# Performance work log

Measured on AMD Instinct MI355X. Metric: run time of the kernel, lower is better.

The kernel has to match this reference:

```python
import jax, jax.numpy as jnp
import numpy as np

D_MODEL = 1024
N_HEADS = 16
HEAD_DIM = D_MODEL // N_HEADS
Q_PROJ = D_MODEL // 2
KV_PROJ = D_MODEL
INIT_SCALE = 0.02
EPS = 1e-5


def _ln(x, g, b):
    mu = jnp.mean(x, axis=-1, keepdims=True)
    var = jnp.mean(jnp.square(x - mu), axis=-1, keepdims=True)
    return (x - mu) * jax.lax.rsqrt(var + EPS) * g + b


def setup_inputs() -> dict:
    key = jax.random.key(0)
    ks = jax.random.split(key, 8)
    B, S = 2, 2048
    x = jax.random.normal(ks[0], (B, S, D_MODEL), dtype=jnp.float32)
    W_dq = INIT_SCALE * jax.random.normal(ks[1], (D_MODEL, Q_PROJ), dtype=jnp.float32)
    W_uq = INIT_SCALE * jax.random.normal(ks[2], (Q_PROJ, D_MODEL), dtype=jnp.float32)
    W_dkv = INIT_SCALE * jax.random.normal(ks[3], (D_MODEL, KV_PROJ), dtype=jnp.float32)
    W_ukv = INIT_SCALE * jax.random.normal(ks[4], (KV_PROJ, 2 * D_MODEL), dtype=jnp.float32)
    wo = INIT_SCALE * jax.random.normal(ks[5], (D_MODEL, D_MODEL), dtype=jnp.float32)
    return {
        "x": x,
        "W_dq": W_dq, "W_uq": W_uq,
        "q_ln_g": jnp.ones((Q_PROJ,), jnp.float32), "q_ln_b": jnp.zeros((Q_PROJ,), jnp.float32),
        "W_dkv": W_dkv, "W_ukv": W_ukv,
        "kv_ln_g": jnp.ones((KV_PROJ,), jnp.float32), "kv_ln_b": jnp.zeros((KV_PROJ,), jnp.float32),
        "preq_g": jnp.ones((D_MODEL,), jnp.float32), "preq_b": jnp.zeros((D_MODEL,), jnp.float32),
        "prekv_g": jnp.ones((D_MODEL,), jnp.float32), "prekv_b": jnp.zeros((D_MODEL,), jnp.float32),
        "wo": wo,
    }


def reference(x, W_dq, W_uq, q_ln_g, q_ln_b, W_dkv, W_ukv, kv_ln_g, kv_ln_b,
              preq_g, preq_b, prekv_g, prekv_b, wo):
    B, S, D = x.shape
    H, dh = N_HEADS, HEAD_DIM
    # Q path: pre-norm -> low-rank down -> LN -> up
    x_q = _ln(x, preq_g, preq_b)
    cq = _ln(x_q @ W_dq, q_ln_g, q_ln_b)            # [B,S,D/2]
    Q = (cq @ W_uq).reshape(B, S, H, dh)             # [B,S,H,dh]
    Q = Q / jnp.sqrt(jnp.asarray(dh, x.dtype))
    # KV path: pre-norm -> compress -> LN -> up, split into K,V
    x_kv = _ln(x, prekv_g, prekv_b)
    ckv = _ln(x_kv @ W_dkv, kv_ln_g, kv_ln_b)        # [B,S,D]
    KV = ckv @ W_ukv                                 # [B,S,2D]
    K, V = jnp.split(KV, 2, axis=-1)
    K = K.reshape(B, S, H, dh)
    V = V.reshape(B, S, H, dh)
    # causal attention (scores materialized as in original)
    scores = jnp.einsum('bqhd,bkhd->bhqk', Q, K)     # [B,H,S,S]
    causal = jnp.tril(jnp.ones((S, S), dtype=bool))  # True where allowed
    scores = jnp.where(causal[None, None], scores, jnp.asarray(-jnp.inf, scores.dtype))
    attn = jax.nn.softmax(scores, axis=-1)
    out = jnp.einsum('bhqk,bkhd->bqhd', attn, V).reshape(B, S, D)
    return out @ wo.T
```

## Files before the change

kernel.cpp:

```cpp
#include <hip/hip_runtime.h>
#include <hip/hip_bf16.h>

#define SEQ   2048
#define BATCH 2
#define NROWS 4096
#define DM    1024
#define NHEAD 16
#define DH    64
#define QP    512
#define KVP   1024
#define CH    8

typedef unsigned short us;
typedef ushort4 us4;
using bf16x8 = __attribute__((ext_vector_type(8))) __bf16;
using f32x4  = __attribute__((ext_vector_type(4))) float;

__device__ __forceinline__ us f2bf(float f) {
  union { __hip_bfloat16 h; us u; } cv;
  cv.h = __float2bfloat16(f);
  return cv.u;
}
__device__ __forceinline__ float bf2f(us u) {
  union { unsigned int u32; float f; } cv;
  cv.u32 = ((unsigned int)u) << 16;
  return cv.f;
}
__device__ __forceinline__ float loadp(const void* p, long i, int isbf) {
  return isbf ? bf2f(((const us*)p)[i]) : ((const float*)p)[i];
}
__device__ __forceinline__ void async16(const void* g, void* l) {
  __builtin_amdgcn_global_load_lds((__attribute__((address_space(1))) void*)g,
                                   (__attribute__((address_space(3))) void*)l,
                                   16, 0, 0);
}
__device__ __forceinline__ unsigned cvtpk(float lo, float hi) {
  unsigned r;
  asm("v_cvt_pk_bf16_f32 %0, %1, %2" : "=v"(r) : "v"(lo), "v"(hi));
  return r;
}

__global__ void detect_dtype(const us* __restrict__ xu, int* __restrict__ flag) {
  __shared__ int red[256];
  const int tid = threadIdx.x;
  int cnt = 0;
  for (int i = tid; i < 4096; i += 256) {
    const int e = (xu[i] >> 7) & 0xff;
    if (e == 0 || (e >= 100 && e <= 134)) cnt++;
  }
  red[tid] = cnt;
  __syncthreads();
  for (int s = 128; s; s >>= 1) {
    if (tid < s) red[tid] += red[tid + s];
    __syncthreads();
  }
  if (tid == 0) *flag = (red[0] >= 3900) ? 1 : 0;
}

struct TD { const void* in; us* out; int R, C, nt, trans; };

__global__ __launch_bounds__(256) void stage0(
    TD t0, TD t1, TD t2, TD t3, TD t4,
    float4* __restrict__ zp, int n4,
    const void* __restrict__ xin,
    const void* __restrict__ g1, const void* __restrict__ b1,
    const void* __restrict__ g2, const void* __restrict__ b2,
    us* __restrict__ out1, us* __restrict__ out2,
    const int* __restrict__ flag)
{
  __shared__ us tile[32][33];
  __shared__ float red[8];
  __shared__ float musd[2];
  const int tid = threadIdx.x;
  const int isbf = *flag;
  int lin = blockIdx.x;

  if (lin < 5120) {
    TD t = t0;
    if (lin >= t.nt) { lin -= t.nt; t = t1;
      if (lin >= t.nt) { lin -= t.nt; t = t2;
        if (lin >= t.nt) { lin -= t.nt; t = t3;
          if (lin >= t.nt) { lin -= t.nt; t = t4; } } } }
    const int ntx = t.C >> 5;
    const int by = lin / ntx, bx = lin - by * ntx;
    const int tx = tid & 31, ty = tid >> 5;
    const long r0 = (long)by * 32, c0 = (long)bx * 32;
    if (t.trans) {
#pragma unroll
      for (int i = 0; i < 32; i += 8)
        tile[ty + i][tx] = isbf ? ((const us*)t.in)[(r0 + ty + i) * t.C + c0 + tx]
                                : f2bf(((const float*)t.in)[(r0 + ty + i) * t.C + c0 + tx]);
      __syncthreads();
#pragma unroll
      for (int i = 0; i < 32; i += 8)
        t.out[(c0 + ty + i) * t.R + r0 + tx] = tile[tx][ty + i];
    } else {
#pragma unroll
      for (int i = 0; i < 32; i += 8)
        t.out[(r0 + ty + i) * t.C + c0 + tx] =
            isbf ? ((const us*)t.in)[(r0 + ty + i) * t.C + c0 + tx]
                 : f2bf(((const float*)t.in)[(r0 + ty + i) * t.C + c0 + tx]);
    }
    return;
  }
  if (lin < 6144) {
    const float4 z = {0.f, 0.f, 0.f, 0.f};
    for (int i = (lin - 5120) * 256 + tid; i < n4; i += 1024 * 256) zp[i] = z;
    return;
  }
  const long row = lin - 6144;
  float v[4];
  float s = 0.f, s2 = 0.f;
#pragma unroll
  for (int i = 0; i < 4; i++) {
    const long c = tid + i * 256;
    const float t = loadp(xin, row * 1024 + c, isbf);
    v[i] = t; s += t; s2 += t * t;
  }
#pragma unroll
  for (int off = 32; off > 0; off >>= 1) {
    s  += __shfl_down(s,  off);
    s2 += __shfl_down(s2, off);
  }
  const int wave = tid >> 6, lane = tid & 63;
  if (lane == 0) { red[wave] = s; red[4 + wave] = s2; }
  __syncthreads();
  if (tid == 0) {
    const float ts = red[0] + red[1] + red[2] + red[3];
    const float t2 = red[4] + red[5] + red[6] + red[7];
    const float mu = ts * (1.f / 1024.f);
    const float var = t2 * (1.f / 1024.f) - mu * mu;
    musd[0] = mu; musd[1] = rsqrtf(var + 1e-5f);
  }
  __syncthreads();
  const float mu = musd[0], rs = musd[1];
#pragma unroll
  for (int i = 0; i < 4; i++) {
    const long c = tid + i * 256;
    const float nrm = (v[i] - mu) * rs;
    out1[row * 1024 + c] = f2bf(nrm * loadp(g1, c, isbf) + loadp(b1, c, isbf));
    out2[row * 1024 + c] = f2bf(nrm * loadp(g2, c, isbf) + loadp(b2, c, isbf));
  }
}

template<int C>
__device__ __forceinline__ void ln_body(const us* __restrict__ in,
                                        const void* __restrict__ g, const void* __restrict__ b,
                                        us* __restrict__ out, long row, int tid, int isbf) {
  constexpr int NP = C / 256;
  float v[NP];
  float s = 0.f, s2 = 0.f;
#pragma unroll
  for (int i = 0; i < NP; i++) {
    const float t = bf2f(in[row * C + tid + i * 256]);
    v[i] = t; s += t; s2 += t * t;
  }
#pragma unroll
  for (int off = 32; off > 0; off >>= 1) {
    s  += __shfl_down(s,  off);
    s2 += __shfl_down(s2, off);
  }
  __shared__ float red[8];
  __shared__ float musd[2];
  const int wave = tid >> 6, lane = tid & 63;
  if (lane == 0) { red[wave] = s; red[4 + wave] = s2; }
  __syncthreads();
  if (tid == 0) {
    const float ts = red[0] + red[1] + red[2] + red[3];
    const float t2 = red[4] + red[5] + red[6] + red[7];
    const float mu = ts * (1.f / C);
    const float var = t2 * (1.f / C) - mu * mu;
    musd[0] = mu; musd[1] = rsqrtf(var + 1e-5f);
  }
  __syncthreads();
  const float mu = musd[0], rs = musd[1];
#pragma unroll
  for (int i = 0; i < NP; i++) {
    const long c = tid + i * 256;
    out[row * C + c] = f2bf((v[i] - mu) * rs * loadp(g, c, isbf) + loadp(b, c, isbf));
  }
}

__global__ __launch_bounds__(256) void ln_rows_pair(
    const us* __restrict__ inq, const void* __restrict__ qg, const void* __restrict__ qb,
    us* __restrict__ outq,
    const us* __restrict__ inkv, const void* __restrict__ kvg, const void* __restrict__ kvb,
    us* __restrict__ outkv,
    const int* __restrict__ flag)
{
  const int isbf = *flag;
  if (blockIdx.x < NROWS)
    ln_body<512>(inq, qg, qb, outq, blockIdx.x, threadIdx.x, isbf);
  else
    ln_body<1024>(inkv, kvg, kvb, outkv, blockIdx.x - NROWS, threadIdx.x, isbf);
}

struct GD { const us* A; const us* Bt; void* C; int N, K, nxs; float scale; int omode; };

__global__ __launch_bounds__(256) void gemm_mt(GD g0, GD g1, int nb0,
                                               const int* __restrict__ flag) {
  __shared__ us As[2][128 * 32];
  __shared__ us Bs[2][128 * 32];
  GD g;
  int lin = blockIdx.x;
  if (lin < nb0) g = g0; else { g = g1; lin -= nb0; }
  const int by = lin >> g.nxs;
  const int bx = lin - (by << g.nxs);
  const int N = g.N, K = g.K;

  const int tid  = threadIdx.x;
  const int lane = tid & 63;
  const int wave = tid >> 6;
  const int n16  = lane & 15;
  const int quad = lane >> 4;
  const long m0 = (long)by * 128;
  const long n0 = (long)bx * 128;
  const int wm = (wave >> 1) * 64;
  const int wn = (wave & 1) * 64;

  const f32x4 zero = {0.f, 0.f, 0.f, 0.f};
  f32x4 acc[4][4];
#pragma unroll
  for (int i = 0; i < 4; i++)
#pragma unroll
    for (int j = 0; j < 4; j++) acc[i][j] = zero;

  const int srow = tid >> 2;
  const int scol = (tid & 3) * 8;
  const us* Ag0 = g.A  + (m0 + srow) * K + scol;
  const us* Ag1 = g.A  + (m0 + 64 + srow) * K + scol;
  const us* Bg0 = g.Bt + (n0 + srow) * K + scol;
  const us* Bg1 = g.Bt + (n0 + 64 + srow) * K + scol;
  const int lds_off = srow * 32 + scol;

  for (int k0 = 0; k0 < K; k0 += 64) {
#pragma unroll
    for (int s = 0; s < 2; s++) {
      const int ks = k0 + s * 32;
      async16(Ag0 + ks, As[s] + lds_off);
      async16(Ag1 + ks, As[s] + 2048 + lds_off);
      async16(Bg0 + ks, Bs[s] + lds_off);
      async16(Bg1 + ks, Bs[s] + 2048 + lds_off);
    }
    __syncthreads();
#pragma unroll
    for (int s = 0; s < 2; s++) {
      bf16x8 af[4], bfv[4];
#pragma unroll
      for (int i = 0; i < 4; i++)
        af[i] = *(const bf16x8*)(As[s] + (wm + i * 16 + n16) * 32 + quad * 8);
#pragma unroll
      for (int j = 0; j < 4; j++)
        bfv[j] = *(const bf16x8*)(Bs[s] + (wn + j * 16 + n16) * 32 + quad * 8);
#pragma unroll
      for (int i = 0; i < 4; i++)
#pragma unroll
        for (int j = 0; j < 4; j++)
          acc[i][j] = __builtin_amdgcn_mfma_f32_16x16x32_bf16(af[i], bfv[j], acc[i][j], 0, 0, 0);
    }
    __syncthreads();
  }

  const bool obf = (g.omode == 1) || (g.omode == 2 && *flag != 0);
  float* Cf = (float*)g.C;
  us* Cb = (us*)g.C;
#pragma unroll
  for (int i = 0; i < 4; i++) {
    const long row = m0 + wm + i * 16 + quad * 4;
#pragma unroll
    for (int j = 0; j < 4; j++) {
      const long col = n0 + wn + j * 16 + n16;
#pragma unroll
      for (int r = 0; r < 4; r++) {
        const float v = acc[i][j][r] * g.scale;
        if (obf) Cb[(row + r) * N + col] = f2bf(v);
        else     Cf[(row + r) * N + col] = v;
      }
    }
  }
}

#define SWZ(row, col) ((row) * 64 + ((col) ^ (((row) & 7) << 3)))

__global__ __launch_bounds__(256, 4) void flash_attn(
    const us* __restrict__ Q, const us* __restrict__ KV,
    float* __restrict__ Oacc, float* __restrict__ Lacc)
{
  __shared__ us Ks[64 * 64];
  __shared__ us Vt[64 * 64];

  int lin = blockIdx.x;
  int qt = 31, nc = 0;
  for (; qt >= 0; --qt) { nc = (qt >> 3) + 1; if (lin < nc) break; lin -= nc; }
  const int chunk = lin;
  const int kt0 = chunk * CH;
  const int kt1 = min(kt0 + CH, qt + 1);

  const int h   = blockIdx.y;
  const int bb  = blockIdx.z;
  const int tid = threadIdx.x;
  const int lane = tid & 63;
  const int wave = tid >> 6;
  const int n16 = lane & 15;
  const int quad = lane >> 4;
  const int qbase = qt * 64;
  const long rowQ0 = (long)bb * SEQ;

  bf16x8 aq[2];
  {
    const long gq = (rowQ0 + qbase + wave * 16 + n16) * DM + h * DH;
    aq[0] = *(const bf16x8*)(Q + gq + quad * 8);
    aq[1] = *(const bf16x8*)(Q + gq + 32 + quad * 8);
  }

  const f32x4 zero = {0.f, 0.f, 0.f, 0.f};
  f32x4 oacc[4];
#pragma unroll
  for (int d = 0; d < 4; d++) oacc[d] = zero;
  float rsum = 0.f;

  const int kk_key = tid >> 3;
  const int kk_d8  = (tid & 7) * 8;
  const int vd  = tid & 63;
  const int vw  = tid >> 6;
  const int vkb = vw * 8;

  const us* kgb = KV + (rowQ0 + kk_key) * 2048 + h * DH + kk_d8;
  const us* vgb = KV + (rowQ0 + vw * 4) * 2048 + KVP + h * DH + vd;

  uint4 kpre0, kpre1;
  us vraw[16];
  auto loadKV = [&](int kt) {
    const us* kg = kgb + (long)kt * (64 * 2048);
    kpre0 = *(const uint4*)kg;
    kpre1 = *(const uint4*)(kg + 32 * 2048);
    const us* vg = vgb + (long)kt * (64 * 2048);
#pragma unroll
    for (int r = 0; r < 4; r++) {
      vraw[r]      = vg[r * 2048];
      vraw[4 + r]  = vg[(16 + r) * 2048];
      vraw[8 + r]  = vg[(32 + r) * 2048];
      vraw[12 + r] = vg[(48 + r) * 2048];
    }
  };
  loadKV(kt0);

  for (int kt = kt0; kt < kt1; kt++) {
    __syncthreads();
    *(uint4*)(Ks + SWZ(kk_key, kk_d8))      = kpre0;
    *(uint4*)(Ks + SWZ(kk_key + 32, kk_d8)) = kpre1;
    {
      uint4 p0, p1;
      p0.x = (unsigned)vraw[0]  | ((unsigned)vraw[1]  << 16);
      p0.y = (unsigned)vraw[2]  | ((unsigned)vraw[3]  << 16);
      p0.z = (unsigned)vraw[4]  | ((unsigned)vraw[5]  << 16);
      p0.w = (unsigned)vraw[6]  | ((unsigned)vraw[7]  << 16);
      p1.x = (unsigned)vraw[8]  | ((unsigned)vraw[9]  << 16);
      p1.y = (unsigned)vraw[10] | ((unsigned)vraw[11] << 16);
      p1.z = (unsigned)vraw[12] | ((unsigned)vraw[13] << 16);
      p1.w = (unsigned)vraw[14] | ((unsigned)vraw[15] << 16);
      *(uint4*)(Vt + SWZ(vd, vkb))      = p0;
      *(uint4*)(Vt + SWZ(vd, vkb + 32)) = p1;
    }
    __syncthreads();
    if (kt + 1 < kt1) loadKV(kt + 1);

    f32x4 sv[4];
#pragma unroll
    for (int j = 0; j < 4; j++) {
      const bf16x8 ak0 = *(const bf16x8*)(Ks + SWZ(j * 16 + n16, quad * 8));
      const bf16x8 ak1 = *(const bf16x8*)(Ks + SWZ(j * 16 + n16, 32 + quad * 8));
      f32x4 s = zero;
      s = __builtin_amdgcn_mfma_f32_16x16x32_bf16(ak0, aq[0], s, 0, 0, 0);
      s = __builtin_amdgcn_mfma_f32_16x16x32_bf16(ak1, aq[1], s, 0, 0, 0);
      sv[j] = s;
    }

    if (kt == qt) {
      const int qrl = wave * 16 + n16;
#pragma unroll
      for (int j = 0; j < 4; j++) {
        const int kl = j * 16 + quad * 4;
#pragma unroll
        for (int r = 0; r < 4; r++)
          sv[j][r] = (kl + r <= qrl) ? sv[j][r] : -1e30f;
      }
    }

    unsigned pep[4][2];
#pragma unroll
    for (int j = 0; j < 4; j++) {
      const float p0 = __builtin_amdgcn_exp2f(sv[j][0]);
      const float p1 = __builtin_amdgcn_exp2f(sv[j][1]);
      const float p2 = __builtin_amdgcn_exp2f(sv[j][2]);
      const float p3 = __builtin_amdgcn_exp2f(sv[j][3]);
      rsum += (p0 + p1) + (p2 + p3);
      pep[j][0] = cvtpk(p0, p1);
      pep[j][1] = cvtpk(p2, p3);
    }

    __builtin_amdgcn_s_setprio(1);
#pragma unroll
    for (int kc = 0; kc < 2; kc++) {
      union { bf16x8 v; unsigned u[4]; } apu;
      apu.u[0] = pep[2 * kc][0];
      apu.u[1] = pep[2 * kc][1];
      apu.u[2] = pep[2 * kc + 1][0];
      apu.u[3] = pep[2 * kc + 1][1];
#pragma unroll
      for (int d = 0; d < 4; d++) {
        const bf16x8 bv = *(const bf16x8*)(Vt + SWZ(d * 16 + n16, kc * 32 + quad * 8));
        oacc[d] = __builtin_amdgcn_mfma_f32_16x16x32_bf16(apu.v, bv, oacc[d], 0, 0, 0);
      }
    }
    __builtin_amdgcn_s_setprio(0);
  }

  rsum += __shfl_xor(rsum, 16);
  rsum += __shfl_xor(rsum, 32);

  const long rw0 = rowQ0 + qbase + wave * 16;
  if (quad == 0)
    atomicAdd(&Lacc[(rw0 + n16) * NHEAD + h], rsum);
#pragma unroll
  for (int r = 0; r < 4; r++) {
    float* dst = Oacc + (rw0 + quad * 4 + r) * DM + h * DH + n16;
#pragma unroll
    for (int d = 0; d < 4; d++)
      atomicAdd(dst + d * 16, oacc[d][r]);
  }
}

__global__ __launch_bounds__(256) void flash_combine(
    const float* __restrict__ Oacc, const float* __restrict__ Lacc,
    us* __restrict__ O)
{
  __shared__ float invl[NHEAD];
  const long row = blockIdx.x;
  const int tid = threadIdx.x;
  if (tid < NHEAD) invl[tid] = 1.f / Lacc[row * NHEAD + tid];
  __syncthreads();
#pragma unroll
  for (int i = 0; i < 4; i++) {
    const int col = tid + i * 256;
    O[row * DM + col] = f2bf(Oacc[row * DM + col] * invl[col >> 6]);
  }
}

extern "C" void kernel_launch(void* const* d_in, const int* in_sizes, int n_in,
                              void* d_out, int out_size, void* d_ws, size_t ws_size,
                              hipStream_t stream) {
  const void* x      = d_in[0];
  const void* Wdq    = d_in[1];
  const void* Wuq    = d_in[2];
  const void* qg     = d_in[3];
  const void* qb     = d_in[4];
  const void* Wdkv   = d_in[5];
  const void* Wukv   = d_in[6];
  const void* kvg    = d_in[7];
  const void* kvb    = d_in[8];
  const void* preqg  = d_in[9];
  const void* preqb  = d_in[10];
  const void* prekvg = d_in[11];
  const void* prekvb = d_in[12];
  const void* wo     = d_in[13];

  char* ws = (char*)d_ws;
  const long MB = 1 << 20;
  int* flag   = (int*)ws;
  us* wdq_t   = (us*)(ws + 1 * MB);
  us* wuq_t   = (us*)(ws + 2 * MB);
  us* wdkv_t  = (us*)(ws + 3 * MB);
  us* wukv_t  = (us*)(ws + 5 * MB);
  us* wo_c    = (us*)(ws + 9 * MB);
  us* xq      = (us*)(ws + 11 * MB);
  us* xkv     = (us*)(ws + 19 * MB);
  float* Oacc = (float*)(ws + 27 * MB);
  float* Lacc = (float*)(ws + 43 * MB);
  us* obuf    = (us*)(ws + 43 * MB + 256 * 1024);
  us* tq_bf   = obuf;
  us* cq      = (us*)(ws + 43 * MB + 256 * 1024 + 8 * MB);
  us* qbuf    = (us*)(ws + 43 * MB + 256 * 1024 + 12 * MB);
  us* tkv_bf  = qbuf;
  us* ckv     = (us*)(ws + 43 * MB + 256 * 1024 + 20 * MB);
  us* kv      = (us*)(ws + 43 * MB + 256 * 1024 + 28 * MB);

  detect_dtype<<<1, 256, 0, stream>>>((const us*)x, flag);

  {
    TD t0 = { Wdq,  wdq_t,  1024,  512,  512, 1 };
    TD t1 = { Wuq,  wuq_t,   512, 1024,  512, 1 };
    TD t2 = { Wdkv, wdkv_t, 1024, 1024, 1024, 1 };
    TD t3 = { Wukv, wukv_t, 1024, 2048, 2048, 1 };
    TD t4 = { wo,   wo_c,   1024, 1024, 1024, 0 };
    const int n4 = (16 * 1024 * 1024 + 256 * 1024) / 16;
    stage0<<<10240, 256, 0, stream>>>(t0, t1, t2, t3, t4,
                                      (float4*)Oacc, n4,
                                      x, preqg, preqb, prekvg, prekvb, xq, xkv, flag);
  }

  {
    GD g0 = { xq,  wdq_t,  tq_bf,   512, 1024, 2, 1.f, 1 };
    GD g1 = { xkv, wdkv_t, tkv_bf, 1024, 1024, 3, 1.f, 1 };
    gemm_mt<<<384, 256, 0, stream>>>(g0, g1, 128, flag);
  }

  ln_rows_pair<<<2 * NROWS, 256, 0, stream>>>(tq_bf, qg, qb, cq, tkv_bf, kvg, kvb, ckv, flag);

  {
    GD g0 = { cq,  wuq_t,  qbuf, 1024,  512, 3, 0.125f * 1.44269504f, 1 };
    GD g1 = { ckv, wukv_t, kv,   2048, 1024, 4, 1.f, 1 };
    gemm_mt<<<768, 256, 0, stream>>>(g0, g1, 256, flag);
  }

  flash_attn<<<dim3(80, NHEAD, BATCH), 256, 0, stream>>>(qbuf, kv, Oacc, Lacc);
  flash_combine<<<NROWS, 256, 0, stream>>>(Oacc, Lacc, obuf);

  {
    GD g0 = { obuf, wo_c, d_out, 1024, 1024, 3, 1.f, 2 };
    gemm_mt<<<256, 256, 0, stream>>>(g0, g0, 256, flag);
  }
}
```

Before: 271.3 us.

## Process 128 query rows per attention block and remap GEMM block order

The attention kernel now has each wave handle two 16-row query groups, so a block covers 128 query rows. Each K/V tile staged in shared memory is reused across twice as many queries, and the atomic partial-sum traffic per key is halved. The causal mask is applied per group only when a tile overlaps the diagonal. The GEMM kernel also permutes block indices in strides of eight, probably so neighbouring tiles land on the same chiplet for cache locality. The cost is higher register pressure, fewer blocks in the attention grid, and coarser causal load balance.

```diff
diff --git a/kernel.cpp b/kernel.cpp
--- a/kernel.cpp
+++ b/kernel.cpp
@@ -203,6 +203,10 @@
   __shared__ us Bs[2][128 * 32];
   GD g;
   int lin = blockIdx.x;
+  {
+    const int cpx = gridDim.x >> 3;
+    lin = (lin & 7) * cpx + (lin >> 3);
+  }
   if (lin < nb0) g = g0; else { g = g1; lin -= nb0; }
   const int by = lin >> g.nxs;
   const int bx = lin - (by << g.nxs);
@@ -290,11 +294,15 @@
   __shared__ us Vt[64 * 64];
 
   int lin = blockIdx.x;
-  int qt = 31, nc = 0;
-  for (; qt >= 0; --qt) { nc = (qt >> 3) + 1; if (lin < nc) break; lin -= nc; }
-  const int chunk = lin;
-  const int kt0 = chunk * CH;
-  const int kt1 = min(kt0 + CH, qt + 1);
+  int qt = 15, nkt = 0, nc = 0;
+  for (; qt >= 0; --qt) {
+    nkt = 2 * qt + 2;
+    nc = (nkt + 7) >> 3;
+    if (lin < nc) break;
+    lin -= nc;
+  }
+  const int kt0 = lin * CH;
+  const int kt1 = min(kt0 + CH, nkt);
 
   const int h   = blockIdx.y;
   const int bb  = blockIdx.z;
@@ -303,21 +311,24 @@
   const int wave = tid >> 6;
   const int n16 = lane & 15;
   const int quad = lane >> 4;
-  const int qbase = qt * 64;
+  const int qbase = qt * 128;
   const long rowQ0 = (long)bb * SEQ;
 
-  bf16x8 aq[2];
-  {
-    const long gq = (rowQ0 + qbase + wave * 16 + n16) * DM + h * DH;
-    aq[0] = *(const bf16x8*)(Q + gq + quad * 8);
-    aq[1] = *(const bf16x8*)(Q + gq + 32 + quad * 8);
+  bf16x8 aq[2][2];
+#pragma unroll
+  for (int g = 0; g < 2; g++) {
+    const long gq = (rowQ0 + qbase + wave * 32 + g * 16 + n16) * DM + h * DH;
+    aq[g][0] = *(const bf16x8*)(Q + gq + quad * 8);
+    aq[g][1] = *(const bf16x8*)(Q + gq + 32 + quad * 8);
   }
 
   const f32x4 zero = {0.f, 0.f, 0.f, 0.f};
-  f32x4 oacc[4];
-#pragma unroll
-  for (int d = 0; d < 4; d++) oacc[d] = zero;
-  float rsum = 0.f;
+  f32x4 oacc[2][4];
+#pragma unroll
+  for (int g = 0; g < 2; g++)
+#pragma unroll
+    for (int d = 0; d < 4; d++) oacc[g][d] = zero;
+  float rsum[2] = {0.f, 0.f};
 
   const int kk_key = tid >> 3;
   const int kk_d8  = (tid & 7) * 8;
@@ -365,69 +376,73 @@
     __syncthreads();
     if (kt + 1 < kt1) loadKV(kt + 1);
 
-    f32x4 sv[4];
+    const int kb = kt << 6;
+    unsigned pep[2][4][2];
+
 #pragma unroll
     for (int j = 0; j < 4; j++) {
       const bf16x8 ak0 = *(const bf16x8*)(Ks + SWZ(j * 16 + n16, quad * 8));
       const bf16x8 ak1 = *(const bf16x8*)(Ks + SWZ(j * 16 + n16, 32 + quad * 8));
-      f32x4 s = zero;
-      s = __builtin_amdgcn_mfma_f32_16x16x32_bf16(ak0, aq[0], s, 0, 0, 0);
-      s = __builtin_amdgcn_mfma_f32_16x16x32_bf16(ak1, aq[1], s, 0, 0, 0);
-      sv[j] = s;
-    }
-
-    if (kt == qt) {
-      const int qrl = wave * 16 + n16;
-#pragma unroll
-      for (int j = 0; j < 4; j++) {
-        const int kl = j * 16 + quad * 4;
-#pragma unroll
-        for (int r = 0; r < 4; r++)
-          sv[j][r] = (kl + r <= qrl) ? sv[j][r] : -1e30f;
+#pragma unroll
+      for (int g = 0; g < 2; g++) {
+        f32x4 s = zero;
+        s = __builtin_amdgcn_mfma_f32_16x16x32_bf16(ak0, aq[g][0], s, 0, 0, 0);
+        s = __builtin_amdgcn_mfma_f32_16x16x32_bf16(ak1, aq[g][1], s, 0, 0, 0);
+        const int qrow0 = qbase + wave * 32 + g * 16;
+        if (kb + 63 > qrow0) {
+          const int qrl = qrow0 + n16 - kb;
+          const int kl = j * 16 + quad * 4;
+#pragma unroll
+          for (int r = 0; r < 4; r++)
+            s[r] = (kl + r <= qrl) ? s[r] : -1e30f;
+        }
+        const float p0 = __builtin_amdgcn_exp2f(s[0]);
+        const float p1 = __builtin_amdgcn_exp2f(s[1]);
+        const float p2 = __builtin_amdgcn_exp2f(s[2]);
+        const float p3 = __builtin_amdgcn_exp2f(s[3]);
+        rsum[g] += (p0 + p1) + (p2 + p3);
+        pep[g][j][0] = cvtpk(p0, p1);
+        pep[g][j][1] = cvtpk(p2, p3);
       }
     }
 
-    unsigned pep[4][2];
-#pragma unroll
-    for (int j = 0; j < 4; j++) {
-      const float p0 = __builtin_amdgcn_exp2f(sv[j][0]);
-      const float p1 = __builtin_amdgcn_exp2f(sv[j][1]);
-      const float p2 = __builtin_amdgcn_exp2f(sv[j][2]);
-      const float p3 = __builtin_amdgcn_exp2f(sv[j][3]);
-      rsum += (p0 + p1) + (p2 + p3);
-      pep[j][0] = cvtpk(p0, p1);
-      pep[j][1] = cvtpk(p2, p3);
-    }
-
     __builtin_amdgcn_s_setprio(1);
 #pragma unroll
     for (int kc = 0; kc < 2; kc++) {
-      union { bf16x8 v; unsigned u[4]; } apu;
-      apu.u[0] = pep[2 * kc][0];
-      apu.u[1] = pep[2 * kc][1];
-      apu.u[2] = pep[2 * kc + 1][0];
-      apu.u[3] = pep[2 * kc + 1][1];
+      union { bf16x8 v; unsigned u[4]; } apu0, apu1;
+      apu0.u[0] = pep[0][2 * kc][0];
+      apu0.u[1] = pep[0][2 * kc][1];
+      apu0.u[2] = pep[0][2 * kc + 1][0];
+      apu0.u[3] = pep[0][2 * kc + 1][1];
+      apu1.u[0] = pep[1][2 * kc][0];
+      apu1.u[1] = pep[1][2 * kc][1];
+      apu1.u[2] = pep[1][2 * kc + 1][0];
+      apu1.u[3] = pep[1][2 * kc + 1][1];
 #pragma unroll
       for (int d = 0; d < 4; d++) {
         const bf16x8 bv = *(const bf16x8*)(Vt + SWZ(d * 16 + n16, kc * 32 + quad * 8));
-        oacc[d] = __builtin_amdgcn_mfma_f32_16x16x32_bf16(apu.v, bv, oacc[d], 0, 0, 0);
+        oacc[0][d] = __builtin_amdgcn_mfma_f32_16x16x32_bf16(apu0.v, bv, oacc[0][d], 0, 0, 0);
+        oacc[1][d] = __builtin_amdgcn_mfma_f32_16x16x32_bf16(apu1.v, bv, oacc[1][d], 0, 0, 0);
       }
     }
     __builtin_amdgcn_s_setprio(0);
   }
 
-  rsum += __shfl_xor(rsum, 16);
-  rsum += __shfl_xor(rsum, 32);
-
-  const long rw0 = rowQ0 + qbase + wave * 16;
-  if (quad == 0)
-    atomicAdd(&Lacc[(rw0 + n16) * NHEAD + h], rsum);
-#pragma unroll
-  for (int r = 0; r < 4; r++) {
-    float* dst = Oacc + (rw0 + quad * 4 + r) * DM + h * DH + n16;
-#pragma unroll
-    for (int d = 0; d < 4; d++)
-      atomicAdd(dst + d * 16, oacc[d][r]);
+#pragma unroll
+  for (int g = 0; g < 2; g++) {
+    float rs = rsum[g];
+    rs += __shfl_xor(rs, 16);
+    rs += __shfl_xor(rs, 32);
+    const long rw0 = rowQ0 + qbase + wave * 32 + g * 16;
+    if (quad == 0)
+      atomicAdd(&Lacc[(rw0 + n16) * NHEAD + h], rs);
+#pragma unroll
+    for (int r = 0; r < 4; r++) {
+      float* dst = Oacc + (rw0 + quad * 4 + r) * DM + h * DH + n16;
+#pragma unroll
+      for (int d = 0; d < 4; d++)
+        atomicAdd(dst + d * 16, oacc[g][d][r]);
+    }
   }
 }
 
@@ -513,7 +528,7 @@
     gemm_mt<<<768, 256, 0, stream>>>(g0, g1, 256, flag);
   }
 
-  flash_attn<<<dim3(80, NHEAD, BATCH), 256, 0, stream>>>(qbuf, kv, Oacc, Lacc);
+  flash_attn<<<dim3(40, NHEAD, BATCH), 256, 0, stream>>>(qbuf, kv, Oacc, Lacc);
   flash_combine<<<NROWS, 256, 0, stream>>>(Oacc, Lacc, obuf);
 
   {
```

Result: slower. 342.3 us (+26.2%).
